# Performance work log

Measured on AMD Instinct MI355X. Metric: run time of the kernel, lower is better.

Reference implementation:

```python
import jax, jax.numpy as jnp
import numpy as np

D_MODEL = 1024
N_HEAD = 16
HEAD_DIM = D_MODEL // N_HEAD

def setup_inputs() -> dict:
    key = jax.random.key(0)
    k1, k2, k3 = jax.random.split(key, 3)
    x = jax.random.normal(k1, (2, 2048, D_MODEL), dtype=jnp.float32)
    # torch Linear weights: [out_features, in_features]; scale like default init
    w_in = jax.random.normal(k2, (3 * D_MODEL, D_MODEL), dtype=jnp.float32) * (1.0 / np.sqrt(D_MODEL))
    w_out = jax.random.normal(k3, (D_MODEL, D_MODEL), dtype=jnp.float32) * (1.0 / np.sqrt(D_MODEL))
    return {"x": x, "w_in": w_in, "w_out": w_out}

def reference(x, w_in, w_out):
    B, T, D = x.shape
    qkv = jnp.einsum('btd,ed->bte', x, w_in)  # [B,T,3D]
    q, k, v = jnp.split(qkv, 3, axis=2)
    def heads(t):
        return t.reshape(B, T, N_HEAD, HEAD_DIM).transpose(0, 2, 1, 3)  # [B,H,T,hd]
    q, k, v = heads(q), heads(k), heads(v)
    att = jnp.einsum('bhqd,bhkd->bhqk', q, k) / np.sqrt(HEAD_DIM).astype(np.float32)
    # NOTE: original uses .tril() (zeroing, NOT -inf) before softmax — faithful reproduction
    causal = jnp.tril(jnp.ones((T, T), dtype=bool))
    att = jnp.where(causal, att, 0.0)
    att = jax.nn.softmax(att, axis=-1)
    out = jnp.einsum('bhqk,bhkd->bhqd', att, v)
    out = out.transpose(0, 2, 1, 3).reshape(B, T, D)
    return jnp.einsum('btd,ed->bte', out, w_out)
```

## Files before the change

### kernel.cpp

```cpp
#include <hip/hip_runtime.h>
#include <hip/hip_bf16.h>
#include <stdint.h>

#define TSEQ   2048
#define DMODEL 1024
#define NHEAD  16
#define HDIM   64

typedef __attribute__((ext_vector_type(8))) __bf16 bf16x8;
typedef __attribute__((ext_vector_type(4))) float f32x4;
typedef __attribute__((ext_vector_type(8))) unsigned short u16x8;

#define SC_LOG2E 0.18033688011112042f

#if __has_builtin(__builtin_amdgcn_exp2f)
#define EXP2F(x) __builtin_amdgcn_exp2f(x)
#else
#define EXP2F(x) __expf(0.6931471805599453f * (x))
#endif

__device__ __forceinline__ unsigned short f2bf(float f) {
    __hip_bfloat16 h = __float2bfloat16(f);
    return __builtin_bit_cast(unsigned short, h);
}
__device__ __forceinline__ float bf2f(unsigned short u) {
    union { unsigned int i; float f; } v;
    v.i = ((unsigned int)u) << 16;
    return v.f;
}

__device__ __forceinline__ void gld_lds16(const void* g, void* s) {
    __builtin_amdgcn_global_load_lds(
        (__attribute__((address_space(1))) void*)(void*)g,
        (__attribute__((address_space(3))) void*)s, 16, 0, 0);
}

#define NX4  (4096 * 1024 / 4)
#define NWI4 (3072 * 1024 / 4)
#define NWO4 (1024 * 1024 / 4)
__global__ void cast3_kernel(const float* __restrict__ x,
                             const float* __restrict__ wi,
                             const float* __restrict__ wo,
                             unsigned short* __restrict__ ox,
                             unsigned short* __restrict__ owi,
                             unsigned short* __restrict__ owo) {
    int i = blockIdx.x * blockDim.x + threadIdx.x;
    const float* s;
    unsigned short* d;
    int off;
    if (i < NX4)              { s = x;  d = ox;  off = i; }
    else if (i < NX4 + NWI4)  { s = wi; d = owi; off = i - NX4; }
    else                      { s = wo; d = owo; off = i - NX4 - NWI4; }
    float4 v = ((const float4*)s)[off];
    ushort4 u;
    u.x = f2bf(v.x); u.y = f2bf(v.y); u.z = f2bf(v.z); u.w = f2bf(v.w);
    ((ushort4*)d)[off] = u;
}

template<bool STORE_F32>
__global__ __launch_bounds__(256, 2)
void gemm_bt(const unsigned short* __restrict__ A,
             const unsigned short* __restrict__ B,
             void* __restrict__ C, int M, int N, int K) {
    (void)M;
    __shared__ unsigned short As[128 * 32];
    __shared__ unsigned short Bs[128 * 32];
    const int tid = threadIdx.x;
    const int nb = N >> 7;
    const int bm = blockIdx.x / nb;
    const int bn = blockIdx.x % nb;
    const int w  = tid >> 6, l = tid & 63;
    const int wr = w >> 1,  wc = w & 1;
    const int lr = l & 15,  lg = l >> 4;

    f32x4 acc[4][4] = {};

    const unsigned short* Ab = A + (size_t)bm * 128 * K;
    const unsigned short* Bb = B + (size_t)bn * 128 * K;

    const int c0 = tid, c1 = tid + 256;
    const int ar0 = c0 >> 2, ak0 = (c0 & 3) * 8;
    const int ar1 = c1 >> 2, ak1 = (c1 & 3) * 8;

    for (int kt = 0; kt < K; kt += 32) {
        __syncthreads();
        gld_lds16(Ab + (size_t)ar0 * K + kt + ak0, As + c0 * 8);
        gld_lds16(Ab + (size_t)ar1 * K + kt + ak1, As + c1 * 8);
        gld_lds16(Bb + (size_t)ar0 * K + kt + ak0, Bs + c0 * 8);
        gld_lds16(Bb + (size_t)ar1 * K + kt + ak1, Bs + c1 * 8);
        __syncthreads();

        bf16x8 af[4], bfr[4];
#pragma unroll
        for (int i = 0; i < 4; i++)
            af[i] = *(const bf16x8*)(As + (wr * 64 + i * 16 + lr) * 32 + lg * 8);
#pragma unroll
        for (int i = 0; i < 4; i++)
            bfr[i] = *(const bf16x8*)(Bs + (wc * 64 + i * 16 + lr) * 32 + lg * 8);
#pragma unroll
        for (int mi = 0; mi < 4; mi++)
#pragma unroll
            for (int ni = 0; ni < 4; ni++)
                acc[mi][ni] = __builtin_amdgcn_mfma_f32_16x16x32_bf16(
                    af[mi], bfr[ni], acc[mi][ni], 0, 0, 0);
    }

    const int row0 = bm * 128 + wr * 64;
    const int col0 = bn * 128 + wc * 64;
#pragma unroll
    for (int mi = 0; mi < 4; mi++)
#pragma unroll
        for (int ni = 0; ni < 4; ni++)
#pragma unroll
            for (int r = 0; r < 4; r++) {
                const int row = row0 + mi * 16 + lg * 4 + r;
                const int col = col0 + ni * 16 + lr;
                if (STORE_F32)
                    ((float*)C)[(size_t)row * N + col] = acc[mi][ni][r];
                else
                    ((unsigned short*)C)[(size_t)row * N + col] = f2bf(acc[mi][ni][r]);
            }
}

__global__ __launch_bounds__(256)
void vtran_kernel(const unsigned short* __restrict__ qkv,
                  unsigned short* __restrict__ vtg,
                  float* __restrict__ ts) {
    __shared__ unsigned short T[64][72];
    const int bid = blockIdx.x;
    const int kb_ = bid & 31;
    const int bh  = bid >> 5;
    const int b = bh >> 4, h = bh & 15;
    const int tid = threadIdx.x;

    const int r = tid >> 2, cq = (tid & 3) * 16;
    const unsigned short* src =
        qkv + ((size_t)(b * TSEQ + kb_ * 64 + r)) * 3072 + 2048 + h * 64 + cq;
    u16x8 v0 = *(const u16x8*)src;
    u16x8 v1 = *(const u16x8*)(src + 8);
#pragma unroll
    for (int i = 0; i < 8; i++) T[r][cq + i] = v0[i];
#pragma unroll
    for (int i = 0; i < 8; i++) T[r][cq + 8 + i] = v1[i];
    __syncthreads();

    const int d = tid >> 2, kq = (tid & 3) * 16;
    u16x8 o0, o1;
#pragma unroll
    for (int i = 0; i < 8; i++) o0[i] = T[kq + i][d];
#pragma unroll
    for (int i = 0; i < 8; i++) o1[i] = T[kq + 8 + i][d];
    unsigned short* dst = vtg + ((size_t)bh * 64 + d) * TSEQ + kb_ * 64 + kq;
    *(u16x8*)dst = o0;
    *(u16x8*)(dst + 8) = o1;

    float ps = 0.f;
#pragma unroll
    for (int i = 0; i < 8; i++) ps += bf2f(o0[i]) + bf2f(o1[i]);
    ps += __shfl_xor(ps, 1);
    ps += __shfl_xor(ps, 2);
    if ((tid & 3) == 0)
        ts[((size_t)bh * 32 + kb_) * 64 + d] = ps;
}

__global__ void vsuf2_kernel(const float* __restrict__ ts,
                             float* __restrict__ tsuf) {
    const int bh = blockIdx.x, d = threadIdx.x;
    float acc = 0.f;
    for (int t = 31; t >= 0; --t) {
        tsuf[((size_t)bh * 32 + t) * 64 + d] = acc;
        acc += ts[((size_t)bh * 32 + t) * 64 + d];
    }
}

__global__ __launch_bounds__(256, 2)
void attn_kernel(const unsigned short* __restrict__ qkv,
                 const unsigned short* __restrict__ vtg,
                 const float* __restrict__ tsuf,
                 unsigned short* __restrict__ out) {
    __shared__ __attribute__((aligned(16))) unsigned short Ks[2][4096];
    __shared__ __attribute__((aligned(16))) unsigned short Vs[2][4096];
    __shared__ __attribute__((aligned(16))) unsigned short Pl[4][32 * 72];

    const int tid = threadIdx.x;
    const int w = tid >> 6, l = tid & 63, lr = l & 15, lg = l >> 4;
    const int bid = blockIdx.x;
    const int j  = bid >> 5;
    const int p  = (j < 8) ? j : 23 - j;
    const int bh = (bid & 7) * 4 + ((bid >> 3) & 3);
    const int b = bh >> 4, h = bh & 15;
    const int strip  = (w < 2) ? (31 - p) : p;
    const int lastkt = strip;
    const int ntiles = 32 - p;
    const size_t rowbase = (size_t)b * TSEQ;
    const int qrow0 = strip * 64 + (w & 1) * 32;

    bf16x8 qf[2][2];
#pragma unroll
    for (int mi = 0; mi < 2; mi++) {
        const unsigned short* qp =
            qkv + (rowbase + qrow0 + mi * 16 + lr) * 3072 + h * 64 + lg * 8;
        qf[mi][0] = *(const bf16x8*)qp;
        qf[mi][1] = *(const bf16x8*)(qp + 32);
    }

    const unsigned short* ksrc[2];
    const unsigned short* vsrc[2];
#pragma unroll
    for (int jj = 0; jj < 2; jj++) {
        const int d = tid + jj * 256;
        const int fr = (d >> 7) * 16 + (d & 15);
        const int cc = ((d >> 6) & 1) * 32 + ((d & 63) >> 4) * 8;
        ksrc[jj] = qkv + (rowbase + fr) * 3072 + 1024 + h * 64 + cc;
        vsrc[jj] = vtg + ((size_t)bh * 64 + fr) * TSEQ + cc;
    }

#define STAGE(kt_, bufi) do {                                      \
        const size_t ko_ = (size_t)(kt_) * 64 * 3072;              \
        const int vo_ = (kt_) * 64;                                \
        gld_lds16(ksrc[0] + ko_, &Ks[bufi][tid * 8]);              \
        gld_lds16(ksrc[1] + ko_, &Ks[bufi][tid * 8 + 2048]);       \
        gld_lds16(vsrc[0] + vo_, &Vs[bufi][tid * 8]);              \
        gld_lds16(vsrc[1] + vo_, &Vs[bufi][tid * 8 + 2048]);       \
    } while (0)

    f32x4 o[2][4] = {};
    float rsum[2][4] = {};
    unsigned short* pw = &Pl[w][0];

    STAGE(0, 0);
    __syncthreads();

    int cur = 0;
    for (int kt = 0; kt < ntiles; ++kt) {
        if (kt + 1 < ntiles) STAGE(kt + 1, cur ^ 1);

        if (kt <= lastkt) {
            const unsigned short* kc = Ks[cur];
            const unsigned short* vc = Vs[cur];

            bf16x8 kb[4][2];
#pragma unroll
            for (int f = 0; f < 4; f++) {
                kb[f][0] = *(const bf16x8*)(kc + ((f * 2 + 0) * 64 + l) * 8);
                kb[f][1] = *(const bf16x8*)(kc + ((f * 2 + 1) * 64 + l) * 8);
            }

            float pvv[2][4][4];
            __builtin_amdgcn_s_setprio(1);
#pragma unroll
            for (int mi = 0; mi < 2; mi++)
#pragma unroll
                for (int f = 0; f < 4; f++) {
                    f32x4 z = {0.f, 0.f, 0.f, 0.f};
                    f32x4 s = __builtin_amdgcn_mfma_f32_16x16x32_bf16(qf[mi][0], kb[f][0], z, 0, 0, 0);
                    s = __builtin_amdgcn_mfma_f32_16x16x32_bf16(qf[mi][1], kb[f][1], s, 0, 0, 0);
#pragma unroll
                    for (int r = 0; r < 4; r++) pvv[mi][f][r] = s[r] * SC_LOG2E;
                }
            __builtin_amdgcn_s_setprio(0);

#pragma unroll
            for (int mi = 0; mi < 2; mi++)
#pragma unroll
                for (int f = 0; f < 4; f++) {
                    const int kcol = kt * 64 + f * 16 + lr;
#pragma unroll
                    for (int r = 0; r < 4; r++) {
                        const int qr = qrow0 + mi * 16 + lg * 4 + r;
                        float sv = (kcol > qr) ? 0.f : pvv[mi][f][r];
                        float pp = EXP2F(sv);
                        rsum[mi][r] += pp;
                        pw[(mi * 16 + lg * 4 + r) * 72 + f * 16 + lr] = f2bf(pp);
                    }
                }

            bf16x8 pa[2][2];
#pragma unroll
            for (int mi = 0; mi < 2; mi++) {
                pa[mi][0] = *(const bf16x8*)(pw + (mi * 16 + lr) * 72 + lg * 8);
                pa[mi][1] = *(const bf16x8*)(pw + (mi * 16 + lr) * 72 + 32 + lg * 8);
            }
            bf16x8 vb[4][2];
#pragma unroll
            for (int f2 = 0; f2 < 4; f2++) {
                vb[f2][0] = *(const bf16x8*)(vc + ((f2 * 2 + 0) * 64 + l) * 8);
                vb[f2][1] = *(const bf16x8*)(vc + ((f2 * 2 + 1) * 64 + l) * 8);
            }
            __builtin_amdgcn_s_setprio(1);
#pragma unroll
            for (int mi = 0; mi < 2; mi++)
#pragma unroll
                for (int f2 = 0; f2 < 4; f2++) {
                    o[mi][f2] = __builtin_amdgcn_mfma_f32_16x16x32_bf16(pa[mi][0], vb[f2][0], o[mi][f2], 0, 0, 0);
                    o[mi][f2] = __builtin_amdgcn_mfma_f32_16x16x32_bf16(pa[mi][1], vb[f2][1], o[mi][f2], 0, 0, 0);
                }
            __builtin_amdgcn_s_setprio(0);
        }

        __syncthreads();
        cur ^= 1;
    }
#undef STAGE

#pragma unroll
    for (int d = 1; d < 16; d <<= 1)
#pragma unroll
        for (int mi = 0; mi < 2; mi++)
#pragma unroll
            for (int r = 0; r < 4; r++)
                rsum[mi][r] += __shfl_xor(rsum[mi][r], d);

    const float nmask = (float)((31 - lastkt) * 64);
    const float* tp = tsuf + ((size_t)bh * 32 + lastkt) * 64;
#pragma unroll
    for (int mi = 0; mi < 2; mi++)
#pragma unroll
        for (int r = 0; r < 4; r++) {
            const float inv = 1.f / (rsum[mi][r] + nmask);
#pragma unroll
            for (int f2 = 0; f2 < 4; f2++) {
                float num = o[mi][f2][r] + tp[f2 * 16 + lr];
                out[(rowbase + qrow0 + mi * 16 + lg * 4 + r) * 1024 + h * 64 + f2 * 16 + lr] =
                    f2bf(num * inv);
            }
        }
}

extern "C" void kernel_launch(void* const* d_in, const int* in_sizes, int n_in,
                              void* d_out, int out_size, void* d_ws, size_t ws_size,
                              hipStream_t stream) {
    const float* x     = (const float*)d_in[0];
    const float* w_in  = (const float*)d_in[1];
    const float* w_out = (const float*)d_in[2];

    unsigned short* ws  = (unsigned short*)d_ws;
    unsigned short* xb  = ws;
    unsigned short* wib = xb  + (size_t)4096 * 1024;
    unsigned short* wob = wib + (size_t)3072 * 1024;
    unsigned short* qkv = wob + (size_t)1024 * 1024;
    unsigned short* ao  = qkv + (size_t)4096 * 3072;
    float* tsuf = (float*)(ao + (size_t)4096 * 1024);
    unsigned short* vtg = (unsigned short*)(tsuf + 32 * 32 * 64);
    float* ts = (float*)(vtg + (size_t)32 * 64 * 2048);

    cast3_kernel<<<(NX4 + NWI4 + NWO4) / 256, 256, 0, stream>>>(
        x, w_in, w_out, xb, wib, wob);

    gemm_bt<false><<<(4096 / 128) * (3072 / 128), 256, 0, stream>>>(
        xb, wib, qkv, 4096, 3072, 1024);
    vtran_kernel<<<32 * 32, 256, 0, stream>>>(qkv, vtg, ts);
    vsuf2_kernel<<<32, 64, 0, stream>>>(ts, tsuf);
    attn_kernel<<<512, 256, 0, stream>>>(qkv, vtg, tsuf, ao);
    gemm_bt<true><<<(4096 / 128) * (1024 / 128), 256, 0, stream>>>(
        ao, wob, (float*)d_out, 4096, 1024, 1024);
}
```

Baseline: 122.7 us.

## Triple-buffer K tiles with partial vmcnt waits and restrict causal mask to diagonal tile

K tiles move to a three-deep LDS ring and are prefetched two iterations ahead, while V stays double-buffered one tile ahead. The full __syncthreads is replaced by s_waitcnt vmcnt(2) plus a raw barrier, so the newest K load can stay in flight across iterations. The causal mask comparison now runs only on the diagonal tile instead of every tile. This costs extra LDS, which may hurt occupancy, and adds redundant clamped loads at the tail.

```diff
diff --git a/kernel.cpp b/kernel.cpp
--- a/kernel.cpp
+++ b/kernel.cpp
@@ -178,7 +178,7 @@
                  const unsigned short* __restrict__ vtg,
                  const float* __restrict__ tsuf,
                  unsigned short* __restrict__ out) {
-    __shared__ __attribute__((aligned(16))) unsigned short Ks[2][4096];
+    __shared__ __attribute__((aligned(16))) unsigned short Ks[3][4096];
     __shared__ __attribute__((aligned(16))) unsigned short Vs[2][4096];
     __shared__ __attribute__((aligned(16))) unsigned short Pl[4][32 * 72];
 
@@ -215,29 +215,39 @@
         vsrc[jj] = vtg + ((size_t)bh * 64 + fr) * TSEQ + cc;
     }
 
-#define STAGE(kt_, bufi) do {                                      \
-        const size_t ko_ = (size_t)(kt_) * 64 * 3072;              \
+#define STAGE_V(kt_, bufi) do {                                    \
         const int vo_ = (kt_) * 64;                                \
-        gld_lds16(ksrc[0] + ko_, &Ks[bufi][tid * 8]);              \
-        gld_lds16(ksrc[1] + ko_, &Ks[bufi][tid * 8 + 2048]);       \
         gld_lds16(vsrc[0] + vo_, &Vs[bufi][tid * 8]);              \
         gld_lds16(vsrc[1] + vo_, &Vs[bufi][tid * 8 + 2048]);       \
     } while (0)
+#define STAGE_K(kt_, bufi) do {                                    \
+        const size_t ko_ = (size_t)(kt_) * 64 * 3072;              \
+        gld_lds16(ksrc[0] + ko_, &Ks[bufi][tid * 8]);              \
+        gld_lds16(ksrc[1] + ko_, &Ks[bufi][tid * 8 + 2048]);       \
+    } while (0)
 
     f32x4 o[2][4] = {};
     float rsum[2][4] = {};
     unsigned short* pw = &Pl[w][0];
 
-    STAGE(0, 0);
-    __syncthreads();
-
-    int cur = 0;
+    STAGE_V(0, 0);
+    STAGE_K(0, 0);
+    STAGE_K((1 < ntiles ? 1 : 0), 1);
+    asm volatile("s_waitcnt vmcnt(2)" ::: "memory");
+    __builtin_amdgcn_s_barrier();
+    asm volatile("" ::: "memory");
+
     for (int kt = 0; kt < ntiles; ++kt) {
-        if (kt + 1 < ntiles) STAGE(kt + 1, cur ^ 1);
+        {
+            const int vt_ = (kt + 1 < ntiles) ? kt + 1 : ntiles - 1;
+            const int kt2 = (kt + 2 < ntiles) ? kt + 2 : ntiles - 1;
+            STAGE_V(vt_, (kt + 1) & 1);
+            STAGE_K(kt2, (kt + 2) % 3);
+        }
 
         if (kt <= lastkt) {
-            const unsigned short* kc = Ks[cur];
-            const unsigned short* vc = Vs[cur];
+            const unsigned short* kc = Ks[kt % 3];
+            const unsigned short* vc = Vs[kt & 1];
 
             bf16x8 kb[4][2];
 #pragma unroll
@@ -260,20 +270,30 @@
                 }
             __builtin_amdgcn_s_setprio(0);
 
+            if (kt == lastkt) {
+#pragma unroll
+                for (int mi = 0; mi < 2; mi++)
+#pragma unroll
+                    for (int f = 0; f < 4; f++) {
+                        const int kcol = kt * 64 + f * 16 + lr;
+#pragma unroll
+                        for (int r = 0; r < 4; r++) {
+                            const int qr = qrow0 + mi * 16 + lg * 4 + r;
+                            if (kcol > qr) pvv[mi][f][r] = 0.f;
+                        }
+                    }
+            }
+
 #pragma unroll
             for (int mi = 0; mi < 2; mi++)
 #pragma unroll
-                for (int f = 0; f < 4; f++) {
-                    const int kcol = kt * 64 + f * 16 + lr;
+                for (int f = 0; f < 4; f++)
 #pragma unroll
                     for (int r = 0; r < 4; r++) {
-                        const int qr = qrow0 + mi * 16 + lg * 4 + r;
-                        float sv = (kcol > qr) ? 0.f : pvv[mi][f][r];
-                        float pp = EXP2F(sv);
+                        float pp = EXP2F(pvv[mi][f][r]);
                         rsum[mi][r] += pp;
                         pw[(mi * 16 + lg * 4 + r) * 72 + f * 16 + lr] = f2bf(pp);
                     }
-                }
 
             bf16x8 pa[2][2];
 #pragma unroll
@@ -298,10 +318,12 @@
             __builtin_amdgcn_s_setprio(0);
         }
 
-        __syncthreads();
-        cur ^= 1;
-    }
-#undef STAGE
+        asm volatile("s_waitcnt vmcnt(2)" ::: "memory");
+        __builtin_amdgcn_s_barrier();
+        asm volatile("" ::: "memory");
+    }
+#undef STAGE_V
+#undef STAGE_K
 
 #pragma unroll
     for (int d = 1; d < 16; d <<= 1)
```

After: 135.7 us. +10.6%, slower.

## Split attention into per-strip 128-thread blocks, read V directly into registers

Applied to the files above, without the earlier changes.

The attention kernel now launches one 128-thread block per 64-row query strip instead of pairing a long and a short strip in a 256-thread block. Each block loops only over its own causal key tiles, so it no longer spins idle iterations. V fragments are loaded straight from global memory into registers rather than staged through LDS, and the causal mask is applied only on the diagonal tile. This cuts LDS use and raises the block count, which may help occupancy. In exchange, the explicit long/short load balancing is lost and V loads go unbuffered on the critical path.

```diff
diff --git a/kernel.cpp b/kernel.cpp
--- a/kernel.cpp
+++ b/kernel.cpp
@@ -173,27 +173,23 @@
     }
 }
 
-__global__ __launch_bounds__(256, 2)
+__global__ __launch_bounds__(128, 2)
 void attn_kernel(const unsigned short* __restrict__ qkv,
                  const unsigned short* __restrict__ vtg,
                  const float* __restrict__ tsuf,
                  unsigned short* __restrict__ out) {
     __shared__ __attribute__((aligned(16))) unsigned short Ks[2][4096];
-    __shared__ __attribute__((aligned(16))) unsigned short Vs[2][4096];
-    __shared__ __attribute__((aligned(16))) unsigned short Pl[4][32 * 72];
+    __shared__ __attribute__((aligned(16))) unsigned short Pl[2][32 * 72];
 
     const int tid = threadIdx.x;
     const int w = tid >> 6, l = tid & 63, lr = l & 15, lg = l >> 4;
     const int bid = blockIdx.x;
-    const int j  = bid >> 5;
-    const int p  = (j < 8) ? j : 23 - j;
+    const int strip = 31 - (bid >> 5);
     const int bh = (bid & 7) * 4 + ((bid >> 3) & 3);
     const int b = bh >> 4, h = bh & 15;
-    const int strip  = (w < 2) ? (31 - p) : p;
     const int lastkt = strip;
-    const int ntiles = 32 - p;
     const size_t rowbase = (size_t)b * TSEQ;
-    const int qrow0 = strip * 64 + (w & 1) * 32;
+    const int qrow0 = strip * 64 + w * 32;
 
     bf16x8 qf[2][2];
 #pragma unroll
@@ -204,62 +200,66 @@
         qf[mi][1] = *(const bf16x8*)(qp + 32);
     }
 
-    const unsigned short* ksrc[2];
-    const unsigned short* vsrc[2];
-#pragma unroll
-    for (int jj = 0; jj < 2; jj++) {
-        const int d = tid + jj * 256;
+    const unsigned short* ksrc[4];
+#pragma unroll
+    for (int jj = 0; jj < 4; jj++) {
+        const int d = tid + jj * 128;
         const int fr = (d >> 7) * 16 + (d & 15);
         const int cc = ((d >> 6) & 1) * 32 + ((d & 63) >> 4) * 8;
         ksrc[jj] = qkv + (rowbase + fr) * 3072 + 1024 + h * 64 + cc;
-        vsrc[jj] = vtg + ((size_t)bh * 64 + fr) * TSEQ + cc;
-    }
-
-#define STAGE(kt_, bufi) do {                                      \
+    }
+    const unsigned short* vb0 = vtg + (size_t)bh * 64 * TSEQ;
+
+#define STAGE_K(kt_, bufi) do {                                    \
         const size_t ko_ = (size_t)(kt_) * 64 * 3072;              \
-        const int vo_ = (kt_) * 64;                                \
         gld_lds16(ksrc[0] + ko_, &Ks[bufi][tid * 8]);              \
-        gld_lds16(ksrc[1] + ko_, &Ks[bufi][tid * 8 + 2048]);       \
-        gld_lds16(vsrc[0] + vo_, &Vs[bufi][tid * 8]);              \
-        gld_lds16(vsrc[1] + vo_, &Vs[bufi][tid * 8 + 2048]);       \
+        gld_lds16(ksrc[1] + ko_, &Ks[bufi][(tid + 128) * 8]);      \
+        gld_lds16(ksrc[2] + ko_, &Ks[bufi][(tid + 256) * 8]);      \
+        gld_lds16(ksrc[3] + ko_, &Ks[bufi][(tid + 384) * 8]);      \
     } while (0)
 
     f32x4 o[2][4] = {};
     float rsum[2][4] = {};
     unsigned short* pw = &Pl[w][0];
 
-    STAGE(0, 0);
+    STAGE_K(0, 0);
     __syncthreads();
 
-    int cur = 0;
-    for (int kt = 0; kt < ntiles; ++kt) {
-        if (kt + 1 < ntiles) STAGE(kt + 1, cur ^ 1);
-
-        if (kt <= lastkt) {
-            const unsigned short* kc = Ks[cur];
-            const unsigned short* vc = Vs[cur];
-
-            bf16x8 kb[4][2];
+    for (int kt = 0; kt <= lastkt; ++kt) {
+        if (kt < lastkt) STAGE_K(kt + 1, (kt + 1) & 1);
+
+        bf16x8 vt[4][2];
+#pragma unroll
+        for (int f2 = 0; f2 < 4; f2++) {
+            const unsigned short* vp =
+                vb0 + (size_t)(f2 * 16 + lr) * TSEQ + kt * 64 + lg * 8;
+            vt[f2][0] = *(const bf16x8*)vp;
+            vt[f2][1] = *(const bf16x8*)(vp + 32);
+        }
+
+        const unsigned short* kc = Ks[kt & 1];
+        bf16x8 kb[4][2];
+#pragma unroll
+        for (int f = 0; f < 4; f++) {
+            kb[f][0] = *(const bf16x8*)(kc + ((f * 2 + 0) * 64 + l) * 8);
+            kb[f][1] = *(const bf16x8*)(kc + ((f * 2 + 1) * 64 + l) * 8);
+        }
+
+        float pvv[2][4][4];
+        __builtin_amdgcn_s_setprio(1);
+#pragma unroll
+        for (int mi = 0; mi < 2; mi++)
 #pragma unroll
             for (int f = 0; f < 4; f++) {
-                kb[f][0] = *(const bf16x8*)(kc + ((f * 2 + 0) * 64 + l) * 8);
-                kb[f][1] = *(const bf16x8*)(kc + ((f * 2 + 1) * 64 + l) * 8);
+                f32x4 z = {0.f, 0.f, 0.f, 0.f};
+                f32x4 s = __builtin_amdgcn_mfma_f32_16x16x32_bf16(qf[mi][0], kb[f][0], z, 0, 0, 0);
+                s = __builtin_amdgcn_mfma_f32_16x16x32_bf16(qf[mi][1], kb[f][1], s, 0, 0, 0);
+#pragma unroll
+                for (int r = 0; r < 4; r++) pvv[mi][f][r] = s[r] * SC_LOG2E;
             }
-
-            float pvv[2][4][4];
-            __builtin_amdgcn_s_setprio(1);
-#pragma unroll
-            for (int mi = 0; mi < 2; mi++)
-#pragma unroll
-                for (int f = 0; f < 4; f++) {
-                    f32x4 z = {0.f, 0.f, 0.f, 0.f};
-                    f32x4 s = __builtin_amdgcn_mfma_f32_16x16x32_bf16(qf[mi][0], kb[f][0], z, 0, 0, 0);
-                    s = __builtin_amdgcn_mfma_f32_16x16x32_bf16(qf[mi][1], kb[f][1], s, 0, 0, 0);
-#pragma unroll
-                    for (int r = 0; r < 4; r++) pvv[mi][f][r] = s[r] * SC_LOG2E;
-                }
-            __builtin_amdgcn_s_setprio(0);
-
+        __builtin_amdgcn_s_setprio(0);
+
+        if (kt == lastkt) {
 #pragma unroll
             for (int mi = 0; mi < 2; mi++)
 #pragma unroll
@@ -268,40 +268,41 @@
 #pragma unroll
                     for (int r = 0; r < 4; r++) {
                         const int qr = qrow0 + mi * 16 + lg * 4 + r;
-                        float sv = (kcol > qr) ? 0.f : pvv[mi][f][r];
-                        float pp = EXP2F(sv);
-                        rsum[mi][r] += pp;
-                        pw[(mi * 16 + lg * 4 + r) * 72 + f * 16 + lr] = f2bf(pp);
+                        if (kcol > qr) pvv[mi][f][r] = 0.f;
                     }
                 }
-
-            bf16x8 pa[2][2];
-#pragma unroll
-            for (int mi = 0; mi < 2; mi++) {
-                pa[mi][0] = *(const bf16x8*)(pw + (mi * 16 + lr) * 72 + lg * 8);
-                pa[mi][1] = *(const bf16x8*)(pw + (mi * 16 + lr) * 72 + 32 + lg * 8);
+        }
+
+#pragma unroll
+        for (int mi = 0; mi < 2; mi++)
+#pragma unroll
+            for (int f = 0; f < 4; f++)
+#pragma unroll
+                for (int r = 0; r < 4; r++) {
+                    float pp = EXP2F(pvv[mi][f][r]);
+                    rsum[mi][r] += pp;
+                    pw[(mi * 16 + lg * 4 + r) * 72 + f * 16 + lr] = f2bf(pp);
+                }
+
+        bf16x8 pa[2][2];
+#pragma unroll
+        for (int mi = 0; mi < 2; mi++) {
+            pa[mi][0] = *(const bf16x8*)(pw + (mi * 16 + lr) * 72 + lg * 8);
+            pa[mi][1] = *(const bf16x8*)(pw + (mi * 16 + lr) * 72 + 32 + lg * 8);
+        }
+        __builtin_amdgcn_s_setprio(1);
+#pragma unroll
+        for (int mi = 0; mi < 2; mi++)
+#pragma unroll
+            for (int f2 = 0; f2 < 4; f2++) {
+                o[mi][f2] = __builtin_amdgcn_mfma_f32_16x16x32_bf16(pa[mi][0], vt[f2][0], o[mi][f2], 0, 0, 0);
+                o[mi][f2] = __builtin_amdgcn_mfma_f32_16x16x32_bf16(pa[mi][1], vt[f2][1], o[mi][f2], 0, 0, 0);
             }
-            bf16x8 vb[4][2];
-#pragma unroll
-            for (int f2 = 0; f2 < 4; f2++) {
-                vb[f2][0] = *(const bf16x8*)(vc + ((f2 * 2 + 0) * 64 + l) * 8);
-                vb[f2][1] = *(const bf16x8*)(vc + ((f2 * 2 + 1) * 64 + l) * 8);
-            }
-            __builtin_amdgcn_s_setprio(1);
-#pragma unroll
-            for (int mi = 0; mi < 2; mi++)
-#pragma unroll
-                for (int f2 = 0; f2 < 4; f2++) {
-                    o[mi][f2] = __builtin_amdgcn_mfma_f32_16x16x32_bf16(pa[mi][0], vb[f2][0], o[mi][f2], 0, 0, 0);
-                    o[mi][f2] = __builtin_amdgcn_mfma_f32_16x16x32_bf16(pa[mi][1], vb[f2][1], o[mi][f2], 0, 0, 0);
-                }
-            __builtin_amdgcn_s_setprio(0);
-        }
+        __builtin_amdgcn_s_setprio(0);
 
         __syncthreads();
-        cur ^= 1;
-    }
-#undef STAGE
+    }
+#undef STAGE_K
 
 #pragma unroll
     for (int d = 1; d < 16; d <<= 1)
@@ -351,7 +352,7 @@
         xb, wib, qkv, 4096, 3072, 1024);
     vtran_kernel<<<32 * 32, 256, 0, stream>>>(qkv, vtg, ts);
     vsuf2_kernel<<<32, 64, 0, stream>>>(ts, tsuf);
-    attn_kernel<<<512, 256, 0, stream>>>(qkv, vtg, tsuf, ao);
+    attn_kernel<<<1024, 128, 0, stream>>>(qkv, vtg, tsuf, ao);
     gemm_bt<true><<<(4096 / 128) * (1024 / 128), 256, 0, stream>>>(
         ao, wob, (float*)d_out, 4096, 1024, 1024);
 }
```

Result: slower. 145.4 us (+18.5%).
